# Optimization experiments

Measured on AMD Instinct MI355X. Metric: run time of the kernel, lower is better.

Reference implementation:

```python
import jax, jax.numpy as jnp
import numpy as np

N = 50000
E = 800000
NFEAT = 128
NHID = 64
NCLASS = 40


def setup_inputs() -> dict:
    key = jax.random.key(0)
    ks = jax.random.split(key, 12)
    return {
        "x": jax.random.normal(ks[0], (N, NFEAT), dtype=jnp.float32),
        "M": jax.random.uniform(ks[1], (N, 1), dtype=jnp.float32),
        "AM": jax.random.uniform(ks[2], (N, 1), dtype=jnp.float32),
        "adj_vals": jax.random.uniform(ks[3], (E,), dtype=jnp.float32),
        "adjZ_vals": jax.random.uniform(ks[4], (E,), dtype=jnp.float32),
        "W0": jax.random.normal(ks[5], (NFEAT, NFEAT), dtype=jnp.float32) * (1.414 / np.sqrt(NFEAT)),
        "b0": jnp.zeros((NFEAT,), dtype=jnp.float32),
        "W1": jax.random.normal(ks[6], (NFEAT, NHID), dtype=jnp.float32) * (1.414 / np.sqrt(NFEAT)),
        "b1": jnp.zeros((NHID,), dtype=jnp.float32),
        "W2": jax.random.normal(ks[7], (NHID, NCLASS), dtype=jnp.float32) * (1.0 / np.sqrt(NHID)),
        "b2": jnp.zeros((NCLASS,), dtype=jnp.float32),
        "row": jax.random.randint(ks[8], (E,), 0, N, dtype=jnp.int32),
        "col": jax.random.randint(ks[9], (E,), 0, N, dtype=jnp.int32),
    }


def _spmm(vals, row, col, X, n):
    # sparse (COO) @ dense: out[r] = sum_e vals[e] * X[col[e]] for row[e]==r
    return jax.ops.segment_sum(vals[:, None] * X[col], row, num_segments=n)


def reference(x, M, AM, adj_vals, adjZ_vals, W0, b0, W1, b1, W2, b2, row, col):
    n = x.shape[0]
    # gc0: PaGConv(nfeat->nfeat) on adjZ, then ReLU (dropout is identity in eval)
    h = _spmm(adjZ_vals, row, col, M * x, n) * AM
    h = jax.nn.relu(h @ W0 + b0)
    # gc1: PaGConv(nfeat->nhid) on adjZ, then ReLU
    h = _spmm(adjZ_vals, row, col, M * h, n) * AM
    h = jax.nn.relu(h @ W1 + b1)
    # gc2: plain GConv(nhid->nclass) on adj
    h = _spmm(adj_vals, row, col, h, n)
    h = h @ W2 + b2
    return jax.nn.log_softmax(h, axis=1)
```

## Files before the change

kernel.cpp:

```cpp
#include <hip/hip_runtime.h>
#include <hip/hip_bf16.h>
#include <math.h>


typedef __attribute__((ext_vector_type(8))) short bf16x8;
typedef __attribute__((ext_vector_type(4))) float f32x4;

__device__ __forceinline__ float rl_f(float v, int j) {
    return __builtin_bit_cast(float,
        __builtin_amdgcn_readlane(__builtin_bit_cast(int, v), j));
}
__device__ __forceinline__ int rl_i(int v, int j) {
    return __builtin_amdgcn_readlane(v, j);
}
__device__ __forceinline__ unsigned short f2bf(float f) {
    unsigned u = __builtin_bit_cast(unsigned, f);
    u += 0x7fffu + ((u >> 16) & 1u);
    return (unsigned short)(u >> 16);
}
__device__ __forceinline__ unsigned pack2bf(float lo, float hi) {
    return (unsigned)f2bf(lo) | ((unsigned)f2bf(hi) << 16);
}
__device__ __forceinline__ float bf_lo(unsigned u) {
    return __builtin_bit_cast(float, u << 16);
}
__device__ __forceinline__ float bf_hi(unsigned u) {
    return __builtin_bit_cast(float, u & 0xffff0000u);
}
__device__ __forceinline__ float clampf(float v) {
    return fminf(fmaxf(v, -1e30f), 1e30f);
}


__global__ void prep_wt(const float* __restrict__ W0, const float* __restrict__ W1,
                        const float* __restrict__ W2,
                        unsigned short* __restrict__ wt0, unsigned short* __restrict__ wt1,
                        unsigned short* __restrict__ wt2) {
    int idx = blockIdx.x * 256 + threadIdx.x;
    if (idx < 128 * 128) {
        int nn = idx >> 7, k = idx & 127;
        wt0[idx] = f2bf(W0[k * 128 + nn]);
    }
    idx -= 128 * 128;
    if (idx >= 0 && idx < 64 * 128) {
        int nn = idx >> 7, k = idx & 127;
        wt1[idx] = f2bf(W1[k * 64 + nn]);
    }
    idx -= 64 * 128;
    if (idx >= 0 && idx < 48 * 64) {
        int nn = idx >> 6, k = idx & 63;
        wt2[idx] = (nn < 40) ? f2bf(W2[k * 40 + nn]) : (unsigned short)0;
    }
}


template <int K, int COLS, int NTPAD, bool ABF16, bool MSCALE>
__device__ __forceinline__ void gemm_mfma_body(const void* __restrict__ Asrc,
                                               const float* __restrict__ Mv,
                                               const unsigned short* __restrict__ Wt,
                                               unsigned short* __restrict__ outp,
                                               int n, int bid) {
    constexpr int KS = K / 32;
    const int lane = threadIdx.x & 63;
    const int wid = threadIdx.x >> 6;
    const int m15 = lane & 15;
    const int q = lane >> 4;
    const int rA = bid * 64 + wid * 16 + m15;

    bf16x8 a[KS];
    if constexpr (ABF16) {
        const unsigned short* A = (const unsigned short*)Asrc;
#pragma unroll
        for (int ks = 0; ks < KS; ++ks) {
            uint4 z = make_uint4(0u, 0u, 0u, 0u);
            if (rA < n) z = *(const uint4*)(A + (size_t)rA * K + ks * 32 + q * 8);
            a[ks] = __builtin_bit_cast(bf16x8, z);
        }
    } else {
        const float* A = (const float*)Asrc;
        float m = 1.0f;
        if constexpr (MSCALE) { if (rA < n) m = Mv[rA]; }
#pragma unroll
        for (int ks = 0; ks < KS; ++ks) {
            float4 lo = make_float4(0.f, 0.f, 0.f, 0.f);
            float4 hi = make_float4(0.f, 0.f, 0.f, 0.f);
            if (rA < n) {
                lo = *(const float4*)(A + (size_t)rA * K + ks * 32 + q * 8);
                hi = *(const float4*)(A + (size_t)rA * K + ks * 32 + q * 8 + 4);
            }
            union { bf16x8 v; unsigned short u[8]; } pk;
            pk.u[0] = f2bf(lo.x * m); pk.u[1] = f2bf(lo.y * m);
            pk.u[2] = f2bf(lo.z * m); pk.u[3] = f2bf(lo.w * m);
            pk.u[4] = f2bf(hi.x * m); pk.u[5] = f2bf(hi.y * m);
            pk.u[6] = f2bf(hi.z * m); pk.u[7] = f2bf(hi.w * m);
            a[ks] = pk.v;
        }
    }

#pragma unroll
    for (int nt = 0; nt < NTPAD / 16; ++nt) {
        f32x4 acc = {0.f, 0.f, 0.f, 0.f};
        const int bn = nt * 16 + m15;
#pragma unroll
        for (int ks = 0; ks < KS; ++ks) {
            const uint4 z = *(const uint4*)(Wt + (size_t)bn * K + ks * 32 + q * 8);
            const bf16x8 b = __builtin_bit_cast(bf16x8, z);
            acc = __builtin_amdgcn_mfma_f32_16x16x32_bf16(a[ks], b, acc, 0, 0, 0);
        }
        const int gc = nt * 16 + m15;
#pragma unroll
        for (int rr = 0; rr < 4; ++rr) {
            const int gr = bid * 64 + wid * 16 + q * 4 + rr;
            bool ok = gr < n;
            if constexpr (NTPAD != COLS) ok = ok && (gc < COLS);
            if (ok) outp[(size_t)gr * COLS + gc] = f2bf(clampf(acc[rr]));
        }
    }
}

template <int K, int COLS, int NTPAD, bool ABF16, bool MSCALE>
__launch_bounds__(256)
__global__ void gemm_mfma(const void* __restrict__ A, const float* __restrict__ Mv,
                          const unsigned short* __restrict__ Wt,
                          unsigned short* __restrict__ out, int n) {
    gemm_mfma_body<K, COLS, NTPAD, ABF16, MSCALE>(A, Mv, Wt, out, n, blockIdx.x);
}


__launch_bounds__(256)
__global__ void gemm0_hist(const float* __restrict__ x, const float* __restrict__ Mv,
                           const unsigned short* __restrict__ Wt0,
                           unsigned short* __restrict__ t_buf,
                           const int* __restrict__ row, int* __restrict__ cnt,
                           int* __restrict__ pos_local, int n, int E, int gemmBlocks) {
    const int b = blockIdx.x;
    if (b < gemmBlocks) {
        gemm_mfma_body<128, 128, 128, false, true>(x, Mv, Wt0, t_buf, n, b);
    } else {
        const int e = (b - gemmBlocks) * 256 + threadIdx.x;
        if (e < E) pos_local[e] = atomicAdd(&cnt[row[e]], 1);
    }
}


__global__ void scan_part(const int* __restrict__ cnt, int* __restrict__ out,
                          int* __restrict__ bsums, int n) {
    __shared__ int sdata[256];
    const int t = threadIdx.x;
    const int base = blockIdx.x * 1024 + t * 4;
    int v[4];
#pragma unroll
    for (int i = 0; i < 4; ++i) v[i] = (base + i < n) ? cnt[base + i] : 0;
    int tsum = v[0] + v[1] + v[2] + v[3];
    sdata[t] = tsum;
    __syncthreads();
    for (int off = 1; off < 256; off <<= 1) {
        int x = (t >= off) ? sdata[t - off] : 0;
        __syncthreads();
        sdata[t] += x;
        __syncthreads();
    }
    int run = sdata[t] - tsum;
    if (t == 255) bsums[blockIdx.x] = sdata[t];
#pragma unroll
    for (int i = 0; i < 4; ++i) {
        if (base + i < n) out[base + i] = run;
        run += v[i];
    }
}

__global__ void scan_top(int* __restrict__ bs, int nb) {
    int t = threadIdx.x;
    int orig = (t < nb) ? bs[t] : 0;
    int v = orig;
#pragma unroll
    for (int off = 1; off < 64; off <<= 1) {
        int x = __shfl_up(v, off);
        if (t >= off) v += x;
    }
    if (t < nb) bs[t] = v - orig;
}

__global__ void scan_add(int* __restrict__ rp, const int* __restrict__ bs,
                         int n, int total) {
    int i = blockIdx.x * blockDim.x + threadIdx.x;
    if (i < n) rp[i] += bs[i >> 10];
    if (i == 0) rp[n] = total;
}


__global__ void scatter_kernel(const int* __restrict__ row, const int* __restrict__ col,
                               const float* __restrict__ vA, const float* __restrict__ vZ,
                               const int* __restrict__ rp, const int* __restrict__ pos_local,
                               float* __restrict__ packed, int E) {
    int e = blockIdx.x * blockDim.x + threadIdx.x;
    if (e >= E) return;
    const int pos = rp[row[e]] + pos_local[e];
    float3 pk;
    pk.x = __int_as_float(col[e]);
    pk.y = vZ[e];
    pk.z = vA[e];
    *(float3*)&packed[(size_t)3 * pos] = pk;
}


__launch_bounds__(256)
__global__ void spmm128_kernel(const float* __restrict__ packed,
                               const int* __restrict__ rp, const unsigned short* __restrict__ X,
                               const float* __restrict__ AM, const float* __restrict__ Mv,
                               const float* __restrict__ bias,
                               unsigned short* __restrict__ out, int n) {
    const int lane = threadIdx.x & 63;
    const int r = (int)((blockIdx.x * (unsigned)blockDim.x + threadIdx.x) >> 6);
    if (r >= n) return;
    const int s = __builtin_amdgcn_readfirstlane(rp[r]);
    const int e = __builtin_amdgcn_readfirstlane(rp[r + 1]);

    float acc0 = 0.0f, acc1 = 0.0f;
    for (int base = s; base < e; base += 64) {
        const int nn = min(64, e - base);
        int ci = 0; float vf = 0.0f;
        if (lane < nn) {
            const float3 pk = *(const float3*)&packed[(size_t)3 * (base + lane)];
            ci = __builtin_bit_cast(int, pk.x);
            vf = pk.y;
        }
        int j = 0;
        for (; j + 8 <= nn; j += 8) {
            unsigned u[8];
#pragma unroll
            for (int q = 0; q < 8; ++q) {
                const int cq = rl_i(ci, j + q);
                u[q] = *(const unsigned*)(X + (size_t)cq * 128 + lane * 2);
            }
#pragma unroll
            for (int q = 0; q < 8; ++q) {
                const float vq = rl_f(vf, j + q);
                acc0 += vq * bf_lo(u[q]);
                acc1 += vq * bf_hi(u[q]);
            }
        }
        for (; j < nn; ++j) {
            const int cq = rl_i(ci, j);
            const float vq = rl_f(vf, j);
            const unsigned u = *(const unsigned*)(X + (size_t)cq * 128 + lane * 2);
            acc0 += vq * bf_lo(u);
            acc1 += vq * bf_hi(u);
        }
    }

    const float am = AM[r];
    const float mr = Mv[r];
    const float o0 = fminf(fmaxf((acc0 * am + bias[2 * lane]) * mr, 0.0f), 1e30f);
    const float o1 = fminf(fmaxf((acc1 * am + bias[2 * lane + 1]) * mr, 0.0f), 1e30f);
    ((unsigned*)out)[(size_t)r * 64 + lane] = pack2bf(o0, o1);
}


__launch_bounds__(256)
__global__ void spmm64_kernel(const float* __restrict__ packed,
                              const int* __restrict__ rp, const unsigned short* __restrict__ X,
                              const float* __restrict__ AM, const float* __restrict__ bias,
                              unsigned short* __restrict__ out, int n) {
    const int lane = threadIdx.x & 63;
    const int g = lane >> 5;
    const int ls = lane & 31;
    const int r = (int)((blockIdx.x * (unsigned)blockDim.x + threadIdx.x) >> 6);
    if (r >= n) return;
    const int s = __builtin_amdgcn_readfirstlane(rp[r]);
    const int e = __builtin_amdgcn_readfirstlane(rp[r + 1]);

    float acc0 = 0.0f, acc1 = 0.0f;
    for (int base = s; base < e; base += 64) {
        const int nn = min(64, e - base);
        int ci = 0; float vf = 0.0f;
        if (lane < nn) {
            const float3 pk = *(const float3*)&packed[(size_t)3 * (base + lane)];
            ci = __builtin_bit_cast(int, pk.x);
            vf = pk.y;
        }
        for (int j = 0; j < nn; j += 8) {
#pragma unroll
            for (int q = 0; q < 4; ++q) {
                const int jj = j + 2 * q + g;
                const bool ok = jj < nn;
                const int idx = jj & 63;
                const int c = __shfl(ci, idx);
                const float v = __shfl(vf, idx);
                if (ok) {
                    const unsigned u = *(const unsigned*)(X + (size_t)c * 64 + ls * 2);
                    acc0 += v * bf_lo(u);
                    acc1 += v * bf_hi(u);
                }
            }
        }
    }
    acc0 += __shfl_xor(acc0, 32);
    acc1 += __shfl_xor(acc1, 32);

    if (lane < 32) {
        const float am = AM[r];
        const float o0 = fminf(fmaxf(acc0 * am + bias[2 * ls], 0.0f), 1e30f);
        const float o1 = fminf(fmaxf(acc1 * am + bias[2 * ls + 1], 0.0f), 1e30f);
        ((unsigned*)out)[(size_t)r * 32 + ls] = pack2bf(o0, o1);
    }
}


__launch_bounds__(256)
__global__ void spmm40_kernel(const float* __restrict__ packed,
                              const int* __restrict__ rp, const unsigned short* __restrict__ X,
                              const float* __restrict__ bias,
                              float* __restrict__ out, int n) {
    const int lane = threadIdx.x & 63;
    const int g = lane / 20;
    const int ls = lane - 20 * g;
    const bool active = g < 3;
    const int r = (int)((blockIdx.x * (unsigned)blockDim.x + threadIdx.x) >> 6);
    if (r >= n) return;
    const int s = __builtin_amdgcn_readfirstlane(rp[r]);
    const int e = __builtin_amdgcn_readfirstlane(rp[r + 1]);

    float acc0 = 0.0f, acc1 = 0.0f;
    for (int base = s; base < e; base += 64) {
        const int nn = min(64, e - base);
        int ci = 0; float vf = 0.0f;
        if (lane < nn) {
            const float3 pk = *(const float3*)&packed[(size_t)3 * (base + lane)];
            ci = __builtin_bit_cast(int, pk.x);
            vf = pk.z;
        }
        for (int j = 0; j < nn; j += 12) {
#pragma unroll
            for (int q = 0; q < 4; ++q) {
                const int jj = j + 3 * q + g;
                const bool ok = active && jj < nn;
                const int idx = jj & 63;
                const int c = __shfl(ci, idx);
                const float v = __shfl(vf, idx);
                if (ok) {
                    const unsigned u = *(const unsigned*)(X + (size_t)c * 40 + ls * 2);
                    acc0 += v * bf_lo(u);
                    acc1 += v * bf_hi(u);
                }
            }
        }
    }
    {
        const float a1 = __shfl(acc0, (lane + 20) & 63);
        const float a2 = __shfl(acc0, (lane + 40) & 63);
        const float b1 = __shfl(acc1, (lane + 20) & 63);
        const float b2 = __shfl(acc1, (lane + 40) & 63);
        acc0 += a1 + a2;
        acc1 += b1 + b2;
    }

    const bool own = lane < 20;
    const float vv0 = own ? fminf(fmaxf(acc0 + bias[2 * ls], -1e30f), 1e30f) : -INFINITY;
    const float vv1 = own ? fminf(fmaxf(acc1 + bias[2 * ls + 1], -1e30f), 1e30f) : -INFINITY;
    float mx = fmaxf(vv0, vv1);
#pragma unroll
    for (int off = 32; off > 0; off >>= 1) mx = fmaxf(mx, __shfl_xor(mx, off));
    float sum = own ? (expf(vv0 - mx) + expf(vv1 - mx)) : 0.0f;
#pragma unroll
    for (int off = 32; off > 0; off >>= 1) sum += __shfl_xor(sum, off);
    if (own) {
        const float lse = mx + logf(sum);
        *(float2*)(out + (size_t)r * 40 + ls * 2) = make_float2(vv0 - lse, vv1 - lse);
    }
}


extern "C" void kernel_launch(void* const* d_in, const int* in_sizes, int n_in,
                              void* d_out, int out_size, void* d_ws, size_t ws_size,
                              hipStream_t stream) {
    const float* x    = (const float*)d_in[0];
    const float* M    = (const float*)d_in[1];
    const float* AM   = (const float*)d_in[2];
    const float* adjv = (const float*)d_in[3];
    const float* adjZ = (const float*)d_in[4];
    const float* W0   = (const float*)d_in[5];
    const float* b0   = (const float*)d_in[6];
    const float* W1   = (const float*)d_in[7];
    const float* b1   = (const float*)d_in[8];
    const float* W2   = (const float*)d_in[9];
    const float* b2   = (const float*)d_in[10];
    const int* row    = (const int*)d_in[11];
    const int* col    = (const int*)d_in[12];
    float* out = (float*)d_out;

    const int n = in_sizes[1];
    const int E = in_sizes[3];

    float* t_f   = (float*)d_ws;
    unsigned short* t_buf = (unsigned short*)t_f;
    unsigned short* wt0 = t_buf + (size_t)n * 128;
    unsigned short* wt1 = wt0 + 128 * 128;
    unsigned short* wt2 = wt1 + 64 * 128;
    float* h_f   = t_f + (size_t)n * 128;
    unsigned short* h_buf = (unsigned short*)h_f;
    int* cnt     = (int*)(h_f + (size_t)n * 128);
    int* rp      = cnt + n;
    int* bsums   = rp + (n + 1);
    float* packed = (float*)(bsums + 64);
    int* pos_local = (int*)h_f;

    hipMemsetAsync(cnt, 0, (size_t)n * sizeof(int), stream);
    prep_wt<<<(128 * 128 + 64 * 128 + 48 * 64 + 255) / 256, 256, 0, stream>>>(
        W0, W1, W2, wt0, wt1, wt2);

    const int gemm0Blocks = (n + 63) / 64;
    const int histBlocks  = (E + 255) / 256;
    gemm0_hist<<<gemm0Blocks + histBlocks, 256, 0, stream>>>(x, M, wt0, t_buf, row, cnt,
                                                             pos_local, n, E, gemm0Blocks);

    const int nblk = (n + 1023) >> 10;
    scan_part<<<nblk, 256, 0, stream>>>(cnt, rp, bsums, n);
    scan_top<<<1, 64, 0, stream>>>(bsums, nblk);
    scan_add<<<(n + 255) / 256, 256, 0, stream>>>(rp, bsums, n, E);
    scatter_kernel<<<(E + 255) / 256, 256, 0, stream>>>(row, col, adjv, adjZ, rp,
                                                        pos_local, packed, E);

    const int spmmBlocks = (n + 3) / 4;
    const int gemmBlocks = (n + 63) / 64;

    spmm128_kernel<<<spmmBlocks, 256, 0, stream>>>(packed, rp, t_buf, AM, M, b0, h_buf, n);
    gemm_mfma<128, 64, 64, true, false><<<gemmBlocks, 256, 0, stream>>>(h_buf, nullptr, wt1,
                                                                        t_buf, n);
    spmm64_kernel<<<spmmBlocks, 256, 0, stream>>>(packed, rp, t_buf, AM, b1, h_buf, n);
    gemm_mfma<64, 40, 48, true, false><<<gemmBlocks, 256, 0, stream>>>(h_buf, nullptr, wt2,
                                                                       t_buf, n);
    spmm40_kernel<<<spmmBlocks, 256, 0, stream>>>(packed, rp, t_buf, b2, out, n);
}
```

Measured before the change: 284.0 us.

## Replace global-atomic row histogram with per-chunk LDS histograms and multi-segment scan

Builds the CSR row counts with per-block LDS histograms over edge chunks, packing two 16-bit counters per word and using two passes over the row range, instead of global atomics on a single count array. The scan then turns the per-chunk counts into per-chunk offsets, and scatter adds the chunk offset to each edge's local position. The GEMM0 and histogram no longer share one fused launch, and the memset of the count array is dropped. This is meant to remove global atomic contention, but it adds G×n count traffic, a serial G-length loop per row in the scan, and only G (about 49) histogram blocks.

```diff
diff --git a/kernel.cpp b/kernel.cpp
--- a/kernel.cpp
+++ b/kernel.cpp
@@ -5,6 +5,9 @@
 
 typedef __attribute__((ext_vector_type(8))) short bf16x8;
 typedef __attribute__((ext_vector_type(4))) float f32x4;
+
+#define EPB_LOG2 14
+#define EPB (1 << EPB_LOG2)
 
 __device__ __forceinline__ float rl_f(float v, int j) {
     return __builtin_bit_cast(float,
@@ -128,29 +131,58 @@
 
 
 __launch_bounds__(256)
-__global__ void gemm0_hist(const float* __restrict__ x, const float* __restrict__ Mv,
-                           const unsigned short* __restrict__ Wt0,
-                           unsigned short* __restrict__ t_buf,
-                           const int* __restrict__ row, int* __restrict__ cnt,
-                           int* __restrict__ pos_local, int n, int E, int gemmBlocks) {
-    const int b = blockIdx.x;
-    if (b < gemmBlocks) {
-        gemm_mfma_body<128, 128, 128, false, true>(x, Mv, Wt0, t_buf, n, b);
-    } else {
-        const int e = (b - gemmBlocks) * 256 + threadIdx.x;
-        if (e < E) pos_local[e] = atomicAdd(&cnt[row[e]], 1);
-    }
-}
-
-
-__global__ void scan_part(const int* __restrict__ cnt, int* __restrict__ out,
-                          int* __restrict__ bsums, int n) {
+__global__ void hist_lds(const int* __restrict__ row, int* __restrict__ cnt64,
+                         int* __restrict__ pos_local, int n, int E) {
+    __shared__ int lds[12544];
+    const int g = blockIdx.x;
+    const int t = threadIdx.x;
+    const int e0 = g << EPB_LOG2;
+    const int e1 = min(e0 + EPB, E);
+    const int halfn = (n + 1) >> 1;
+
+    for (int pass = 0; pass < 2; ++pass) {
+        const int rlo = pass * halfn;
+        const int rhi = min(rlo + halfn, n);
+        const int bins = (rhi - rlo + 1) >> 1;
+        for (int i = t; i < bins; i += 256) lds[i] = 0;
+        __syncthreads();
+        for (int e = e0 + t; e < e1; e += 256) {
+            const int r = row[e];
+            if (r >= rlo && r < rhi) {
+                const int lr = r - rlo;
+                const int old = atomicAdd(&lds[lr >> 1], (lr & 1) ? 0x10000 : 1);
+                pos_local[e] = (lr & 1) ? (old >> 16) : (old & 0xffff);
+            }
+        }
+        __syncthreads();
+        for (int i = t; i < rhi - rlo; i += 256) {
+            const int v = lds[i >> 1];
+            cnt64[(size_t)g * n + rlo + i] = (i & 1) ? (v >> 16) : (v & 0xffff);
+        }
+        __syncthreads();
+    }
+}
+
+
+__global__ void scan_part_g(int* __restrict__ cnt64, int* __restrict__ rp,
+                            int* __restrict__ bsums, int n, int G) {
     __shared__ int sdata[256];
     const int t = threadIdx.x;
     const int base = blockIdx.x * 1024 + t * 4;
     int v[4];
 #pragma unroll
-    for (int i = 0; i < 4; ++i) v[i] = (base + i < n) ? cnt[base + i] : 0;
+    for (int i = 0; i < 4; ++i) {
+        const int idx = base + i;
+        int s = 0;
+        if (idx < n) {
+            for (int x = 0; x < G; ++x) {
+                const int c = cnt64[(size_t)x * n + idx];
+                cnt64[(size_t)x * n + idx] = s;
+                s += c;
+            }
+        }
+        v[i] = s;
+    }
     int tsum = v[0] + v[1] + v[2] + v[3];
     sdata[t] = tsum;
     __syncthreads();
@@ -164,7 +196,7 @@
     if (t == 255) bsums[blockIdx.x] = sdata[t];
 #pragma unroll
     for (int i = 0; i < 4; ++i) {
-        if (base + i < n) out[base + i] = run;
+        if (base + i < n) rp[base + i] = run;
         run += v[i];
     }
 }
@@ -191,16 +223,23 @@
 
 __global__ void scatter_kernel(const int* __restrict__ row, const int* __restrict__ col,
                                const float* __restrict__ vA, const float* __restrict__ vZ,
-                               const int* __restrict__ rp, const int* __restrict__ pos_local,
-                               float* __restrict__ packed, int E) {
-    int e = blockIdx.x * blockDim.x + threadIdx.x;
-    if (e >= E) return;
-    const int pos = rp[row[e]] + pos_local[e];
-    float3 pk;
-    pk.x = __int_as_float(col[e]);
-    pk.y = vZ[e];
-    pk.z = vA[e];
-    *(float3*)&packed[(size_t)3 * pos] = pk;
+                               const int* __restrict__ rp, const int* __restrict__ cnt64,
+                               const int* __restrict__ pos_local,
+                               float* __restrict__ packed, int E, int n) {
+    const int base = blockIdx.x * 1024 + threadIdx.x;
+#pragma unroll
+    for (int u = 0; u < 4; ++u) {
+        const int e = base + u * 256;
+        if (e >= E) continue;
+        const int g = e >> EPB_LOG2;
+        const int r = row[e];
+        const int pos = rp[r] + cnt64[(size_t)g * n + r] + pos_local[e];
+        float3 pk;
+        pk.x = __int_as_float(col[e]);
+        pk.y = vZ[e];
+        pk.z = vA[e];
+        *(float3*)&packed[(size_t)3 * pos] = pk;
+    }
 }
 
 
@@ -391,38 +430,35 @@
 
     const int n = in_sizes[1];
     const int E = in_sizes[3];
-
-    float* t_f   = (float*)d_ws;
-    unsigned short* t_buf = (unsigned short*)t_f;
-    unsigned short* wt0 = t_buf + (size_t)n * 128;
-    unsigned short* wt1 = wt0 + 128 * 128;
-    unsigned short* wt2 = wt1 + 64 * 128;
-    float* h_f   = t_f + (size_t)n * 128;
-    unsigned short* h_buf = (unsigned short*)h_f;
-    int* cnt     = (int*)(h_f + (size_t)n * 128);
-    int* rp      = cnt + n;
-    int* bsums   = rp + (n + 1);
-    float* packed = (float*)(bsums + 64);
-    int* pos_local = (int*)h_f;
-
-    hipMemsetAsync(cnt, 0, (size_t)n * sizeof(int), stream);
+    const int G = (E + EPB - 1) >> EPB_LOG2;
+
+    char* p = (char*)d_ws;
+    unsigned short* t_buf = (unsigned short*)p;  p += (size_t)n * 128 * 2;
+    unsigned short* h_buf = (unsigned short*)p;  p += (size_t)n * 128 * 2;
+    unsigned short* wt0   = (unsigned short*)p;  p += 128 * 128 * 2;
+    unsigned short* wt1   = (unsigned short*)p;  p += 64 * 128 * 2;
+    unsigned short* wt2   = (unsigned short*)p;  p += 48 * 64 * 2 + 64;
+    int* cnt64     = (int*)p;                    p += (size_t)G * n * 4;
+    int* rp        = (int*)p;                    p += (size_t)(n + 1) * 4;
+    int* bsums     = (int*)p;                    p += 64 * 4;
+    int* pos_local = (int*)p;                    p += (size_t)E * 4;
+    float* packed  = (float*)p;
+
     prep_wt<<<(128 * 128 + 64 * 128 + 48 * 64 + 255) / 256, 256, 0, stream>>>(
         W0, W1, W2, wt0, wt1, wt2);
 
-    const int gemm0Blocks = (n + 63) / 64;
-    const int histBlocks  = (E + 255) / 256;
-    gemm0_hist<<<gemm0Blocks + histBlocks, 256, 0, stream>>>(x, M, wt0, t_buf, row, cnt,
-                                                             pos_local, n, E, gemm0Blocks);
-
+    const int gemmBlocks = (n + 63) / 64;
+
+    hist_lds<<<G, 256, 0, stream>>>(row, cnt64, pos_local, n, E);
+    gemm_mfma<128, 128, 128, false, true><<<gemmBlocks, 256, 0, stream>>>(x, M, wt0, t_buf, n);
     const int nblk = (n + 1023) >> 10;
-    scan_part<<<nblk, 256, 0, stream>>>(cnt, rp, bsums, n);
+    scan_part_g<<<nblk, 256, 0, stream>>>(cnt64, rp, bsums, n, G);
     scan_top<<<1, 64, 0, stream>>>(bsums, nblk);
     scan_add<<<(n + 255) / 256, 256, 0, stream>>>(rp, bsums, n, E);
-    scatter_kernel<<<(E + 255) / 256, 256, 0, stream>>>(row, col, adjv, adjZ, rp,
-                                                        pos_local, packed, E);
+    scatter_kernel<<<(E + 1023) / 1024, 256, 0, stream>>>(row, col, adjv, adjZ, rp, cnt64,
+                                                          pos_local, packed, E, n);
 
     const int spmmBlocks = (n + 3) / 4;
-    const int gemmBlocks = (n + 63) / 64;
 
     spmm128_kernel<<<spmmBlocks, 256, 0, stream>>>(packed, rp, t_buf, AM, M, b0, h_buf, n);
     gemm_mfma<128, 64, 64, true, false><<<gemmBlocks, 256, 0, stream>>>(h_buf, nullptr, wt1,
```

After: 348.3 us. 1.23x slower.
